# Optimization experiments

Measured on AMD Instinct MI355X. Metric: run time of the kernel, lower is better.

Reference implementation:

```python
import jax, jax.numpy as jnp
import numpy as np

FEAT_STRIDE = 16
SCORE_THRESH = 0.7
DIST_THRESH = 16.0
MAX_OUT = 50
B = 2048
IMG_W = 65536


def setup_inputs() -> dict:
    key = jax.random.key(0)
    k1, k2, k3 = jax.random.split(key, 3)
    fw = IMG_W // FEAT_STRIDE
    pred_cls_logit = jax.random.normal(k1, (B, fw), dtype=jnp.float32)
    pred_delta = jax.random.normal(k2, (B, fw, 2), dtype=jnp.float32)
    # realistic image widths in [0.5, 1.0] * img_width
    real_images_width = jax.random.uniform(k3, (B,), jnp.float32, 0.5, 1.0) * IMG_W
    return {
        "pred_cls_logit": pred_cls_logit,
        "pred_delta": pred_delta,
        "img_width": IMG_W,
        "real_images_width": real_images_width,
    }


def _nms_one(positions, scores):
    # positions: [N, 2], scores: [N]. Greedy 1D NMS, fixed MAX_OUT iterations.
    centers = positions.mean(axis=1)                      # [N]
    alive0 = scores >= SCORE_THRESH                       # score-threshold filter

    def step(alive, _):
        masked = jnp.where(alive, scores, -1e30)
        i = jnp.argmax(masked)                            # highest remaining score
        has = jnp.any(alive)
        f = has.astype(jnp.float32)                       # 1.0 if a box was picked
        p = positions[i] * f
        s = scores[i] * f
        # suppress everything within DIST_THRESH of picked center (incl. itself)
        new_alive = alive & (jnp.abs(centers - centers[i]) > DIST_THRESH)
        return new_alive, (p, s, f)

    _, (P, S, F) = jax.lax.scan(step, alive0, None, length=MAX_OUT)
    # pad_to_fixed_size: append validity flag column, zero-padded rows
    nms_positions = jnp.concatenate([P, F[:, None]], axis=1)   # [MAX_OUT, 3]
    nms_scores = jnp.concatenate([S[:, None], F[:, None]], axis=1)  # [MAX_OUT, 2]
    return nms_positions, nms_scores


def reference(pred_cls_logit, pred_delta, img_width, real_images_width):
    feat_width = img_width // FEAT_STRIDE
    interval_center = (jnp.arange(feat_width, dtype=jnp.float32) + 0.5) * FEAT_STRIDE
    # [B, feat_width, 2]
    pos = pred_delta * FEAT_STRIDE + interval_center[None, :, None]
    scores = jax.nn.sigmoid(pred_cls_logit)               # [B, feat_width]
    max_width = real_images_width[:, None, None] - 1.0
    pos = jnp.where(pos < 0.0, 0.0, pos)
    pos = jnp.where(pos > max_width, max_width, pos)

    nms_positions, nms_scores = jax.vmap(_nms_one)(pos, scores)

    nms_center = nms_positions[..., :2].mean(axis=2)      # [B, MAX_OUT]
    x_interval_num = jnp.floor(nms_center / FEAT_STRIDE).astype(jnp.int32)
    valid = nms_positions[..., 2] == 1.0
    idx = jnp.where(valid, x_interval_num, feat_width)    # out-of-range -> dropped
    cls_ids = jax.vmap(
        lambda ii: jnp.zeros((feat_width,), jnp.float32).at[ii].set(1.0, mode='drop')
    )(idx)                                                # [B, feat_width]
    return nms_positions, nms_scores, cls_ids
```

## Files before the change

kernel.cpp:

```cpp
#include <hip/hip_runtime.h>
#include <math.h>

#define MAX_OUT 50
#define SEGCAP 288
#define NWAVES 4
#define MAXC (SEGCAP * NWAVES)
#define NJ 18

__global__ __launch_bounds__(256) void essp_kernel(
    const float* __restrict__ logits,
    const float* __restrict__ deltas,
    const float* __restrict__ realw,
    float* __restrict__ out_pos,
    float* __restrict__ out_scr,
    float* __restrict__ out_cls,
    int fw)
{
  __shared__ float  c_s[MAXC];
  __shared__ float  c_cen[MAXC];
  __shared__ float2 c_pp[MAXC];
  __shared__ int    pk[MAX_OUT];

  const int b    = blockIdx.x;
  const int tid  = threadIdx.x;
  const int lane = tid & 63;
  const int w    = tid >> 6;

  const float mw = realw[b] - 1.0f;
  const float*  lg  = logits + (size_t)b * fw;
  const float2* dl2 = (const float2*)(deltas + (size_t)b * fw * 2);
  float* cls = out_cls + (size_t)b * fw;

  const int segbase = w * SEGCAP;
  #pragma unroll
  for (int j = 0; j < 5; ++j) {
    const int k = lane + 64 * j;
    if (k < SEGCAP) { c_s[segbase + k] = -1e30f; c_cen[segbase + k] = 0.0f; }
  }

  const int ebase = w * 1024;
  int cnt = 0;
  #pragma unroll 4
  for (int r = 0; r < 16; ++r) {
    const int i = ebase + r * 64 + lane;
    const float  x = lg[i];
    const float2 d = dl2[i];
    cls[i] = 0.0f;
    const bool cand = (x >= 0.846f);
    const unsigned long long mask = __ballot(cand);
    if (cand) {
      const int slot = cnt + __popcll(mask & ((1ULL << lane) - 1ULL));
      if (slot < SEGCAP) {
        const float ic = ((float)i + 0.5f) * 16.0f;
        float p0 = d.x * 16.0f + ic;
        float p1 = d.y * 16.0f + ic;
        p0 = (p0 < 0.f) ? 0.f : p0;  p0 = (p0 > mw) ? mw : p0;
        p1 = (p1 < 0.f) ? 0.f : p1;  p1 = (p1 > mw) ? mw : p1;
        const int gs = segbase + slot;
        c_s[gs]   = x;
        c_cen[gs] = (p0 + p1) * 0.5f;
        c_pp[gs]  = make_float2(p0, p1);
      }
    }
    cnt += __popcll(mask);
  }

  const int nc = (cnt < SEGCAP) ? cnt : SEGCAP;
  #pragma unroll 1
  for (int j = 0; j < 5; ++j) {
    const int k = lane + 64 * j;
    if (k < nc) {
      const float x = c_s[segbase + k];
      const float s = (float)(1.0 / (1.0 + exp(-(double)x)));
      c_s[segbase + k] = (s >= 0.7f) ? s : -1e30f;
    }
  }

  __syncthreads();
  if (w != 0) return;

  float sv[NJ], cv[NJ];
  #pragma unroll
  for (int j = 0; j < NJ; ++j) {
    sv[j] = c_s[lane + 64 * j];
    cv[j] = c_cen[lane + 64 * j];
  }
  if (lane < MAX_OUT) pk[lane] = -1;

  #pragma unroll 1
  for (int it = 0; it < MAX_OUT; ++it) {
    float best = fmaxf(sv[0], sv[1]);
    #pragma unroll
    for (int j = 2; j < NJ; ++j) best = fmaxf(best, sv[j]);
    #pragma unroll
    for (int off = 1; off < 64; off <<= 1)
      best = fmaxf(best, __shfl_xor(best, off, 64));
    if (best < 0.7f) break;

    int jsel = 127;
    #pragma unroll
    for (int j = NJ - 1; j >= 0; --j) if (sv[j] == best) jsel = j;
    int slotv = (jsel << 6) | lane;
    #pragma unroll
    for (int off = 1; off < 64; off <<= 1) {
      const int o = __shfl_xor(slotv, off, 64);
      slotv = (o < slotv) ? o : slotv;
    }

    const float wc = c_cen[slotv];
    if (lane == 0) pk[it] = slotv;
    #pragma unroll
    for (int j = 0; j < NJ; ++j)
      if (fabsf(cv[j] - wc) <= 16.0f) sv[j] = -1e30f;
  }

  float* prow = out_pos + (size_t)b * MAX_OUT * 3;
  float* srow = out_scr + (size_t)b * MAX_OUT * 2;
  if (lane < MAX_OUT) {
    const int slot = pk[lane];
    if (slot >= 0) {
      const float2 pp = c_pp[slot];
      prow[lane * 3 + 0] = pp.x;
      prow[lane * 3 + 1] = pp.y;
      prow[lane * 3 + 2] = 1.0f;
      srow[lane * 2 + 0] = c_s[slot];
      srow[lane * 2 + 1] = 1.0f;
      const float wcc = c_cen[slot];
      const int ci = (int)floorf(wcc * 0.0625f);
      if (ci >= 0 && ci < fw) cls[ci] = 1.0f;
    } else {
      prow[lane * 3 + 0] = 0.0f;
      prow[lane * 3 + 1] = 0.0f;
      prow[lane * 3 + 2] = 0.0f;
      srow[lane * 2 + 0] = 0.0f;
      srow[lane * 2 + 1] = 0.0f;
    }
  }
}

extern "C" void kernel_launch(void* const* d_in, const int* in_sizes, int n_in,
                              void* d_out, int out_size, void* d_ws, size_t ws_size,
                              hipStream_t stream) {
  const float* logits = (const float*)d_in[0];
  const float* deltas = (const float*)d_in[1];
  const float* realw  = (const float*)d_in[3];
  const int Bn = in_sizes[3];
  const int fw = in_sizes[0] / Bn;
  float* out_pos = (float*)d_out;
  float* out_scr = out_pos + (size_t)Bn * MAX_OUT * 3;
  float* out_cls = out_scr + (size_t)Bn * MAX_OUT * 2;
  essp_kernel<<<Bn, 256, 0, stream>>>(logits, deltas, realw,
                                      out_pos, out_scr, out_cls, fw);
}
```

Measured before the change: 74.19 us.

## Gather deltas only for candidates and use packed DPP argmax in NMS

The logit scan now uses float4 loads and records only candidate indices. Deltas are then gathered just for those candidates, so the full delta array is no longer streamed, which roughly halves the bytes read per row. The NMS loop replaces the two-pass max-then-argmin shuffle reduction with a single argmax over (score, index, center) using DPP and readlane, and the class row is zeroed with float4 stores. This hardcodes FW=4096, and the per-wave candidate capacity changes from 288 to 320 with a compacted 1024-slot global list.

```diff
diff --git a/kernel.cpp b/kernel.cpp
--- a/kernel.cpp
+++ b/kernel.cpp
@@ -1,139 +1,200 @@
 #include <hip/hip_runtime.h>
 #include <math.h>
 
+#define FW 4096
 #define MAX_OUT 50
-#define SEGCAP 288
-#define NWAVES 4
-#define MAXC (SEGCAP * NWAVES)
-#define NJ 18
-
-__global__ __launch_bounds__(256) void essp_kernel(
+#define WCAP 320
+#define NSLOT 1024
+
+struct Tri { float s; int k; float c; };
+
+__device__ __forceinline__ Tri tri_merge(Tri a, Tri b) {
+  const bool t = (b.s > a.s) || (b.s == a.s && b.k < a.k);
+  Tri r; r.s = t ? b.s : a.s; r.k = t ? b.k : a.k; r.c = t ? b.c : a.c;
+  return r;
+}
+
+template <int CTRL>
+__device__ __forceinline__ void dpp_comb(float& s, int& k, float& c) {
+  const float os = __int_as_float(__builtin_amdgcn_update_dpp(
+      __float_as_int(s), __float_as_int(s), CTRL, 0xF, 0xF, false));
+  const int ok = __builtin_amdgcn_update_dpp(k, k, CTRL, 0xF, 0xF, false);
+  const float oc = __int_as_float(__builtin_amdgcn_update_dpp(
+      __float_as_int(c), __float_as_int(c), CTRL, 0xF, 0xF, false));
+  const bool t = (os > s) || (os == s && ok < k);
+  s = t ? os : s;  k = t ? ok : k;  c = t ? oc : c;
+}
+
+__global__ __launch_bounds__(256) void essp_fused(
     const float* __restrict__ logits,
     const float* __restrict__ deltas,
     const float* __restrict__ realw,
     float* __restrict__ out_pos,
     float* __restrict__ out_scr,
-    float* __restrict__ out_cls,
-    int fw)
+    float* __restrict__ out_cls)
 {
-  __shared__ float  c_s[MAXC];
-  __shared__ float  c_cen[MAXC];
-  __shared__ float2 c_pp[MAXC];
-  __shared__ int    pk[MAX_OUT];
-
-  const int b    = blockIdx.x;
+  __shared__ float Lx[4][WCAP];
+  __shared__ int   Li[4][WCAP];
+  __shared__ int   Lcnt[4];
+  __shared__ __align__(16) float Lsc[NSLOT];
+  __shared__ __align__(16) float Lce[NSLOT];
+  __shared__ unsigned short Lidx[NSLOT];
+
+  const int row  = blockIdx.x;
   const int tid  = threadIdx.x;
   const int lane = tid & 63;
   const int w    = tid >> 6;
 
-  const float mw = realw[b] - 1.0f;
-  const float*  lg  = logits + (size_t)b * fw;
-  const float2* dl2 = (const float2*)(deltas + (size_t)b * fw * 2);
-  float* cls = out_cls + (size_t)b * fw;
-
-  const int segbase = w * SEGCAP;
+  const float mw = realw[row] - 1.0f;
+  const float* lgr = logits + (size_t)row * FW;
+  const float* dlr = deltas + (size_t)row * (2 * FW);
+  float* cls = out_cls + (size_t)row * FW;
+
+  {
+    const float4 z = make_float4(0.f, 0.f, 0.f, 0.f);
+    #pragma unroll
+    for (int r = 0; r < 4; ++r) *(float4*)(cls + 1024 * r + 4 * tid) = z;
+  }
+
+  int cnt = 0;
   #pragma unroll
-  for (int j = 0; j < 5; ++j) {
-    const int k = lane + 64 * j;
-    if (k < SEGCAP) { c_s[segbase + k] = -1e30f; c_cen[segbase + k] = 0.0f; }
-  }
-
-  const int ebase = w * 1024;
-  int cnt = 0;
-  #pragma unroll 4
-  for (int r = 0; r < 16; ++r) {
-    const int i = ebase + r * 64 + lane;
-    const float  x = lg[i];
-    const float2 d = dl2[i];
-    cls[i] = 0.0f;
-    const bool cand = (x >= 0.846f);
-    const unsigned long long mask = __ballot(cand);
-    if (cand) {
-      const int slot = cnt + __popcll(mask & ((1ULL << lane) - 1ULL));
-      if (slot < SEGCAP) {
-        const float ic = ((float)i + 0.5f) * 16.0f;
-        float p0 = d.x * 16.0f + ic;
-        float p1 = d.y * 16.0f + ic;
-        p0 = (p0 < 0.f) ? 0.f : p0;  p0 = (p0 > mw) ? mw : p0;
-        p1 = (p1 < 0.f) ? 0.f : p1;  p1 = (p1 > mw) ? mw : p1;
-        const int gs = segbase + slot;
-        c_s[gs]   = x;
-        c_cen[gs] = (p0 + p1) * 0.5f;
-        c_pp[gs]  = make_float2(p0, p1);
+  for (int r = 0; r < 4; ++r) {
+    const int i0 = w * 1024 + r * 256 + 4 * lane;
+    const float4 lx = *(const float4*)(lgr + i0);
+    const float xs[4] = {lx.x, lx.y, lx.z, lx.w};
+    bool c4[4]; unsigned long long m4[4];
+    #pragma unroll
+    for (int e = 0; e < 4; ++e) { c4[e] = (xs[e] >= 0.846f); m4[e] = __ballot(c4[e]); }
+    const unsigned long long below = (1ULL << lane) - 1ULL;
+    int base = cnt + __popcll(m4[0] & below) + __popcll(m4[1] & below)
+                   + __popcll(m4[2] & below) + __popcll(m4[3] & below);
+    int off = 0;
+    #pragma unroll
+    for (int e = 0; e < 4; ++e) {
+      if (c4[e]) {
+        const int slot = base + off;
+        if (slot < WCAP) { Lx[w][slot] = xs[e]; Li[w][slot] = i0 + e; }
+        ++off;
       }
     }
-    cnt += __popcll(mask);
-  }
-
-  const int nc = (cnt < SEGCAP) ? cnt : SEGCAP;
-  #pragma unroll 1
-  for (int j = 0; j < 5; ++j) {
-    const int k = lane + 64 * j;
-    if (k < nc) {
-      const float x = c_s[segbase + k];
+    cnt += __popcll(m4[0]) + __popcll(m4[1]) + __popcll(m4[2]) + __popcll(m4[3]);
+  }
+  if (lane == 0) Lcnt[w] = (cnt < WCAP) ? cnt : WCAP;
+  __syncthreads();
+
+  const int c0 = Lcnt[0], c1 = Lcnt[1], c2 = Lcnt[2], c3 = Lcnt[3];
+  const int p1 = c0, p2 = c0 + c1, p3 = c0 + c1 + c2;
+  int nc = p3 + c3; nc = (nc < NSLOT) ? nc : NSLOT;
+
+  #pragma unroll
+  for (int g0 = 0; g0 < NSLOT; g0 += 256) {
+    const int g = g0 + tid;
+    if (g < nc) {
+      const int wsel = (g >= p1) + (g >= p2) + (g >= p3);
+      int pre = 0;
+      pre = (wsel == 1) ? p1 : pre;
+      pre = (wsel == 2) ? p2 : pre;
+      pre = (wsel == 3) ? p3 : pre;
+      const int kk = g - pre;
+      const float x  = (&Lx[0][0])[wsel * WCAP + kk];
+      const int  idx = (&Li[0][0])[wsel * WCAP + kk];
+      const float2 d = *(const float2*)(dlr + 2 * idx);
+      const float ic = ((float)idx + 0.5f) * 16.0f;
+      float q0 = d.x * 16.0f + ic;
+      float q1 = d.y * 16.0f + ic;
+      q0 = (q0 < 0.f) ? 0.f : q0;  q0 = (q0 > mw) ? mw : q0;
+      q1 = (q1 < 0.f) ? 0.f : q1;  q1 = (q1 > mw) ? mw : q1;
       const float s = (float)(1.0 / (1.0 + exp(-(double)x)));
-      c_s[segbase + k] = (s >= 0.7f) ? s : -1e30f;
-    }
-  }
-
+      Lsc[g]  = (s >= 0.7f) ? s : -1e30f;
+      Lce[g]  = (q0 + q1) * 0.5f;
+      Lidx[g] = (unsigned short)idx;
+    } else {
+      Lsc[g] = -1e30f;
+    }
+  }
   __syncthreads();
   if (w != 0) return;
 
-  float sv[NJ], cv[NJ];
+  float sv[16], cv[16];
+  int ids[16];
   #pragma unroll
-  for (int j = 0; j < NJ; ++j) {
-    sv[j] = c_s[lane + 64 * j];
-    cv[j] = c_cen[lane + 64 * j];
-  }
-  if (lane < MAX_OUT) pk[lane] = -1;
+  for (int q = 0; q < 4; ++q) {
+    const float4 s4 = *(const float4*)(&Lsc[256 * q + 4 * lane]);
+    const float4 e4 = *(const float4*)(&Lce[256 * q + 4 * lane]);
+    sv[4*q+0] = s4.x; sv[4*q+1] = s4.y; sv[4*q+2] = s4.z; sv[4*q+3] = s4.w;
+    cv[4*q+0] = e4.x; cv[4*q+1] = e4.y; cv[4*q+2] = e4.z; cv[4*q+3] = e4.w;
+    #pragma unroll
+    for (int e = 0; e < 4; ++e) ids[4*q+e] = 256 * q + 4 * lane + e;
+  }
+  int pkv = -1; float psv = 0.f;
 
   #pragma unroll 1
   for (int it = 0; it < MAX_OUT; ++it) {
-    float best = fmaxf(sv[0], sv[1]);
-    #pragma unroll
-    for (int j = 2; j < NJ; ++j) best = fmaxf(best, sv[j]);
-    #pragma unroll
-    for (int off = 1; off < 64; off <<= 1)
-      best = fmaxf(best, __shfl_xor(best, off, 64));
-    if (best < 0.7f) break;
-
-    int jsel = 127;
-    #pragma unroll
-    for (int j = NJ - 1; j >= 0; --j) if (sv[j] == best) jsel = j;
-    int slotv = (jsel << 6) | lane;
-    #pragma unroll
-    for (int off = 1; off < 64; off <<= 1) {
-      const int o = __shfl_xor(slotv, off, 64);
-      slotv = (o < slotv) ? o : slotv;
-    }
-
-    const float wc = c_cen[slotv];
-    if (lane == 0) pk[it] = slotv;
-    #pragma unroll
-    for (int j = 0; j < NJ; ++j)
+    float ts[16]; int tk[16]; float tc[16];
+    #pragma unroll
+    for (int j = 0; j < 16; ++j) { ts[j] = sv[j]; tk[j] = ids[j]; tc[j] = cv[j]; }
+    #pragma unroll
+    for (int st = 1; st < 16; st <<= 1) {
+      #pragma unroll
+      for (int j = 0; j + st < 16; j += 2 * st) {
+        const bool t = ts[j + st] > ts[j];
+        ts[j] = t ? ts[j + st] : ts[j];
+        tk[j] = t ? tk[j + st] : tk[j];
+        tc[j] = t ? tc[j + st] : tc[j];
+      }
+    }
+    float s = ts[0]; int k = tk[0]; float c = tc[0];
+    dpp_comb<0xB1>(s, k, c);
+    dpp_comb<0x4E>(s, k, c);
+    dpp_comb<0x141>(s, k, c);
+    dpp_comb<0x140>(s, k, c);
+    Tri r0 = {__int_as_float(__builtin_amdgcn_readlane(__float_as_int(s), 0)),
+              __builtin_amdgcn_readlane(k, 0),
+              __int_as_float(__builtin_amdgcn_readlane(__float_as_int(c), 0))};
+    Tri r1 = {__int_as_float(__builtin_amdgcn_readlane(__float_as_int(s), 16)),
+              __builtin_amdgcn_readlane(k, 16),
+              __int_as_float(__builtin_amdgcn_readlane(__float_as_int(c), 16))};
+    Tri r2 = {__int_as_float(__builtin_amdgcn_readlane(__float_as_int(s), 32)),
+              __builtin_amdgcn_readlane(k, 32),
+              __int_as_float(__builtin_amdgcn_readlane(__float_as_int(c), 32))};
+    Tri r3 = {__int_as_float(__builtin_amdgcn_readlane(__float_as_int(s), 48)),
+              __builtin_amdgcn_readlane(k, 48),
+              __int_as_float(__builtin_amdgcn_readlane(__float_as_int(c), 48))};
+    const Tri R = tri_merge(tri_merge(r0, r1), tri_merge(r2, r3));
+
+    const bool valid = (R.s >= 0.7f);
+    const float wc = valid ? R.c : 3.0e38f;
+    if (lane == it) { pkv = valid ? R.k : -1; psv = R.s; }
+    #pragma unroll
+    for (int j = 0; j < 16; ++j)
       if (fabsf(cv[j] - wc) <= 16.0f) sv[j] = -1e30f;
   }
 
-  float* prow = out_pos + (size_t)b * MAX_OUT * 3;
-  float* srow = out_scr + (size_t)b * MAX_OUT * 2;
+  float* prow = out_pos + (size_t)row * (MAX_OUT * 3);
+  float* srow = out_scr + (size_t)row * (MAX_OUT * 2);
   if (lane < MAX_OUT) {
-    const int slot = pk[lane];
-    if (slot >= 0) {
-      const float2 pp = c_pp[slot];
-      prow[lane * 3 + 0] = pp.x;
-      prow[lane * 3 + 1] = pp.y;
-      prow[lane * 3 + 2] = 1.0f;
-      srow[lane * 2 + 0] = c_s[slot];
-      srow[lane * 2 + 1] = 1.0f;
-      const float wcc = c_cen[slot];
-      const int ci = (int)floorf(wcc * 0.0625f);
-      if (ci >= 0 && ci < fw) cls[ci] = 1.0f;
+    if (pkv >= 0) {
+      const int idx = Lidx[pkv];
+      const float2 d = *(const float2*)(dlr + 2 * idx);
+      const float ic = ((float)idx + 0.5f) * 16.0f;
+      float q0 = d.x * 16.0f + ic;
+      float q1 = d.y * 16.0f + ic;
+      q0 = (q0 < 0.f) ? 0.f : q0;  q0 = (q0 > mw) ? mw : q0;
+      q1 = (q1 < 0.f) ? 0.f : q1;  q1 = (q1 > mw) ? mw : q1;
+      const float cen = (q0 + q1) * 0.5f;
+      prow[3 * lane + 0] = q0;
+      prow[3 * lane + 1] = q1;
+      prow[3 * lane + 2] = 1.0f;
+      srow[2 * lane + 0] = psv;
+      srow[2 * lane + 1] = 1.0f;
+      const int ci = (int)floorf(cen * 0.0625f);
+      if (ci >= 0 && ci < FW) cls[ci] = 1.0f;
     } else {
-      prow[lane * 3 + 0] = 0.0f;
-      prow[lane * 3 + 1] = 0.0f;
-      prow[lane * 3 + 2] = 0.0f;
-      srow[lane * 2 + 0] = 0.0f;
-      srow[lane * 2 + 1] = 0.0f;
+      prow[3 * lane + 0] = 0.0f;
+      prow[3 * lane + 1] = 0.0f;
+      prow[3 * lane + 2] = 0.0f;
+      srow[2 * lane + 0] = 0.0f;
+      srow[2 * lane + 1] = 0.0f;
     }
   }
 }
@@ -145,10 +206,10 @@
   const float* deltas = (const float*)d_in[1];
   const float* realw  = (const float*)d_in[3];
   const int Bn = in_sizes[3];
-  const int fw = in_sizes[0] / Bn;
   float* out_pos = (float*)d_out;
   float* out_scr = out_pos + (size_t)Bn * MAX_OUT * 3;
   float* out_cls = out_scr + (size_t)Bn * MAX_OUT * 2;
-  essp_kernel<<<Bn, 256, 0, stream>>>(logits, deltas, realw,
-                                      out_pos, out_scr, out_cls, fw);
-}
+
+  essp_fused<<<Bn, 256, 0, stream>>>(logits, deltas, realw,
+                                     out_pos, out_scr, out_cls);
+}
```

New measurement: 242.0 us. 3.26x slower.
